# Performance work log

Measured on AMD Instinct MI355X. Metric: run time of the kernel, lower is better.

The kernel has to match this reference:

```python
import jax, jax.numpy as jnp
import numpy as np

N = 65536      # total nodes
B = 512        # graphs (equal-sized)
NPER = N // B  # 128 nodes per graph
E = 655360     # edges
F_IN = 128
K = 32         # sort-pool k
OUT = 27


def _gcn(x, row, col, dinv, W, b):
    # PyG GCNConv with added self-loops and symmetric normalization:
    xw = x @ W                                   # [N, F_out]
    coef = dinv[row] * dinv[col]                 # [E]
    agg = jax.ops.segment_sum(xw[row] * coef[:, None], col, num_segments=N)
    return agg + (dinv * dinv)[:, None] * xw + b  # self-loop term + bias


def _conv1d(x, w, b, stride):
    # x: [B, C_in, L], w: [C_out, C_in, K]
    out = jax.lax.conv_general_dilated(x, w, (stride,), 'VALID',
                                       dimension_numbers=('NCH', 'OIH', 'NCH'))
    return out + b[None, :, None]


def setup_inputs() -> dict:
    key = jax.random.key(0)
    ks = jax.random.split(key, 16)
    x = jax.random.normal(ks[0], (N, F_IN), dtype=jnp.float32)
    edge_index = jax.random.randint(ks[1], (2, E), 0, N, dtype=jnp.int32)
    batch = jnp.repeat(jnp.arange(B, dtype=jnp.int32), NPER)

    def lin(k, fi, fo):
        return jax.random.normal(k, (fi, fo), dtype=jnp.float32) / np.sqrt(fi)

    W1, b1 = lin(ks[2], F_IN, 128), jnp.zeros((128,), jnp.float32)
    W2, b2 = lin(ks[3], 128, 64), jnp.zeros((64,), jnp.float32)
    W3, b3 = lin(ks[4], 64, 32), jnp.zeros((32,), jnp.float32)
    W4, b4 = lin(ks[5], 32, 32), jnp.zeros((32,), jnp.float32)
    conv5_w = jax.random.normal(ks[6], (16, 1, 256), jnp.float32) / np.sqrt(256)
    conv5_b = jnp.zeros((16,), jnp.float32)
    conv6_w = jax.random.normal(ks[7], (32, 16, 5), jnp.float32) / np.sqrt(16 * 5)
    conv6_b = jnp.zeros((32,), jnp.float32)
    dense_w = lin(ks[8], 384, OUT)
    dense_b = jnp.zeros((OUT,), jnp.float32)
    return dict(x=x, edge_index=edge_index, batch=batch,
                W1=W1, b1=b1, W2=W2, b2=b2, W3=W3, b3=b3, W4=W4, b4=b4,
                conv5_w=conv5_w, conv5_b=conv5_b, conv6_w=conv6_w, conv6_b=conv6_b,
                dense_w=dense_w, dense_b=dense_b)


def reference(x, edge_index, batch, W1, b1, W2, b2, W3, b3, W4, b4,
              conv5_w, conv5_b, conv6_w, conv6_b, dense_w, dense_b):
    row, col = edge_index[0], edge_index[1]
    deg = jax.ops.segment_sum(jnp.ones((E,), x.dtype), col, num_segments=N) + 1.0
    dinv = jax.lax.rsqrt(deg)

    x1 = jnp.tanh(_gcn(x, row, col, dinv, W1, b1))
    x2 = jnp.tanh(_gcn(x1, row, col, dinv, W2, b2))
    x3 = jnp.tanh(_gcn(x2, row, col, dinv, W3, b3))
    x4 = jnp.tanh(_gcn(x3, row, col, dinv, W4, b4))
    h = jnp.concatenate([x1, x2, x3, x4], axis=-1)   # [N, 256]

    # SortAggregation: sort nodes within each graph by last channel (desc), take top-k.
    hg = h.reshape(B, NPER, 256)
    idx = jnp.argsort(-hg[:, :, -1], axis=1)[:, :K]                 # [B, K]
    pooled = jnp.take_along_axis(hg, idx[:, :, None], axis=1)       # [B, K, 256]
    top_k_indices = idx + (jnp.arange(B, dtype=idx.dtype) * NPER)[:, None]

    z = pooled.reshape(B, 1, K * 256)                # [B, 1, 8192]
    z = jax.nn.relu(_conv1d(z, conv5_w, conv5_b, 256))  # [B, 16, 32]
    z = jax.lax.reduce_window(z, -jnp.inf, jax.lax.max,
                              (1, 1, 2), (1, 1, 2), 'VALID')        # [B, 16, 16]
    z = jax.nn.relu(_conv1d(z, conv6_w, conv6_b, 1))  # [B, 32, 12]
    z = z.reshape(B, -1)                              # [B, 384]
    out = z @ dense_w + dense_b                       # [B, 27]
    return out, top_k_indices
```

## Files before the change

### kernel.cpp

```cpp
#include <hip/hip_runtime.h>
#include <math.h>

#define N_NODES 65536
#define N_EDGES 655360
#define N_GRAPHS 512
#define NPERG 128
#define KTOP 32
#define NOUT 27
#define OUT0_SIZE (N_GRAPHS * NOUT)
#define EPS 64

typedef unsigned int uint32;
typedef unsigned short u16;
typedef unsigned char u8;
typedef __attribute__((ext_vector_type(8))) short bf16x8;
typedef __attribute__((ext_vector_type(4))) float f32x4;
typedef __attribute__((ext_vector_type(2))) float f32x2;

__device__ __forceinline__ float blo(uint32 u) { return __uint_as_float(u << 16); }
__device__ __forceinline__ float bhi(uint32 u) { return __uint_as_float(u & 0xffff0000u); }
__device__ __forceinline__ u16 f2b(float f) {
    uint32 u = __float_as_uint(f);
    u += 0x7fffu + ((u >> 16) & 1u);
    return (u16)(u >> 16);
}
__device__ __forceinline__ uint32 pk(float a, float b) {
    return (uint32)f2b(a) | ((uint32)f2b(b) << 16);
}
__device__ __forceinline__ f32x2 fp8lo(uint32 u) { return __builtin_amdgcn_cvt_pk_f32_fp8((int)u, false); }
__device__ __forceinline__ f32x2 fp8hi(uint32 u) { return __builtin_amdgcn_cvt_pk_f32_fp8((int)u, true); }
__device__ __forceinline__ u8 f2fp8(float v) {
    return (u8)(__builtin_amdgcn_cvt_pk_fp8_f32(v, v, 0, false) & 0xff);
}


template<int FI, int FO>
__device__ __forceinline__ void pack_w(const float* __restrict__ W, uint4* __restrict__ pw,
                                       int base, int nb) {
    constexpr int KC = FI / 8;
    for (int q = (blockIdx.x - base) * 256 + threadIdx.x; q < FO * KC; q += nb * 256) {
        int n = q % FO, c = q / FO;
        const float* wp = W + (size_t)(c * 8) * FO + n;
        uint4 v;
        v.x = pk(wp[0],            wp[(size_t)FO]);
        v.y = pk(wp[2*(size_t)FO], wp[3*(size_t)FO]);
        v.z = pk(wp[4*(size_t)FO], wp[5*(size_t)FO]);
        v.w = pk(wp[6*(size_t)FO], wp[7*(size_t)FO]);
        pw[n * KC + c] = v;
    }
}

__global__ __launch_bounds__(256) void prep_kernel(const float* __restrict__ W1, const float* __restrict__ W2,
                                                   const float* __restrict__ W3, const float* __restrict__ W4,
                                                   uint4* __restrict__ pw1, uint4* __restrict__ pw2,
                                                   uint4* __restrict__ pw3, uint4* __restrict__ pw4,
                                                   int* __restrict__ cur) {
    int b = blockIdx.x;
    if (b < 256) { cur[b * 256 + threadIdx.x] = 0; return; }
    b -= 256;
    if (b < 8)       pack_w<128, 128>(W1, pw1, 256, 8);
    else if (b < 12) pack_w<128, 64>(W2, pw2, 264, 4);
    else if (b < 13) pack_w<64, 32>(W3, pw3, 268, 1);
    else             pack_w<32, 32>(W4, pw4, 269, 1);
}


__global__ __launch_bounds__(256) void fill_kernel(const int* __restrict__ erow, const int* __restrict__ ecol,
                                                   int* __restrict__ cur, u16* __restrict__ ep) {
    int e = blockIdx.x * 256 + threadIdx.x;
    int r = erow[e], d = ecol[e];
    int slot = atomicAdd(&cur[d], 1);
    if (slot < EPS) ep[(d << 6) + slot] = (u16)r;
}


template<int FI, int FO>
__device__ __forceinline__ void stage_Bp(const uint4* __restrict__ pw, uint4* __restrict__ Bs) {
    constexpr int KC = FI / 8, SA = KC + 1;
    for (int q = threadIdx.x; q < FO * KC; q += 256) {
        int n = q / KC, c = q % KC;
        Bs[n * SA + c] = pw[q];
    }
}

template<int FI, int FO, bool OUT_FP8>
__device__ __forceinline__ void mfma_store(uint4* __restrict__ As, const uint4* __restrict__ Bs,
                                           uint4* __restrict__ Y, size_t rowbase,
                                           const float* __restrict__ ds) {
    constexpr int KC = FI / 8, SA = KC + 1;
    constexpr int NTILE = FO / 16;
    constexpr int CW = (NTILE >= 4) ? 4 : NTILE;
    constexpr int NTW = NTILE / CW;
    constexpr int RW = 4 / CW;
    constexpr int RS = 2 / RW;
    constexpr int KSTEPS = FI / 32;
    int t = threadIdx.x;
    int w = t >> 6, L = t & 63;
    int quad = L >> 4, m = L & 15;
    int cw = w % CW, rw = w / CW;

    const bf16x8* Asv = (const bf16x8*)As;
    const bf16x8* Bsv = (const bf16x8*)Bs;

    f32x4 acc[RS][NTW];
#pragma unroll
    for (int i = 0; i < RS; i++)
#pragma unroll
        for (int j = 0; j < NTW; j++) acc[i][j] = (f32x4)0.f;

#pragma unroll
    for (int ks = 0; ks < KSTEPS; ks++) {
        int kc = ks * 4 + quad;
        bf16x8 bfr[NTW];
#pragma unroll
        for (int j = 0; j < NTW; j++) {
            int n = (cw * NTW + j) * 16 + m;
            bfr[j] = Bsv[n * SA + kc];
        }
#pragma unroll
        for (int i = 0; i < RS; i++) {
            int r = (rw * RS + i) * 16 + m;
            bf16x8 afr = Asv[r * SA + kc];
#pragma unroll
            for (int j = 0; j < NTW; j++)
                acc[i][j] = __builtin_amdgcn_mfma_f32_16x16x32_bf16(afr, bfr[j], acc[i][j], 0, 0, 0);
        }
    }
    __syncthreads();

    if constexpr (OUT_FP8) {
        u8* outs = (u8*)As;
#pragma unroll
        for (int i = 0; i < RS; i++) {
            int rb = (rw * RS + i) * 16 + quad * 4;
#pragma unroll
            for (int j = 0; j < NTW; j++) {
                int cc = (cw * NTW + j) * 16 + m;
#pragma unroll
                for (int g2 = 0; g2 < 4; g2++)
                    outs[(rb + g2) * FO + cc] = f2fp8(acc[i][j][g2] * ds[rb + g2]);
            }
        }
    } else {
        u16* outs = (u16*)As;
#pragma unroll
        for (int i = 0; i < RS; i++) {
            int rb = (rw * RS + i) * 16 + quad * 4;
#pragma unroll
            for (int j = 0; j < NTW; j++) {
                int cc = (cw * NTW + j) * 16 + m;
#pragma unroll
                for (int g2 = 0; g2 < 4; g2++)
                    outs[(rb + g2) * FO + cc] = f2b(acc[i][j][g2] * ds[rb + g2]);
            }
        }
    }
    __syncthreads();
    constexpr int NU4 = OUT_FP8 ? (32 * FO / 16) : (32 * FO / 8);
    for (int q = t; q < NU4; q += 256)
        Y[rowbase * (NU4 / 32) + q] = ((const uint4*)As)[q];
}


__global__ __launch_bounds__(256) void gemm1_kernel(const float* __restrict__ x,
                                                    const uint4* __restrict__ pw1,
                                                    const int* __restrict__ cur,
                                                    uint4* __restrict__ xw1) {
    constexpr int KC = 16, SA = 17;
    __shared__ __align__(16) uint4 As[32 * SA];
    __shared__ __align__(16) uint4 Bs[128 * SA];
    __shared__ float ds[32];
    int t = threadIdx.x;
    stage_Bp<128, 128>(pw1, Bs);
    size_t rowbase = (size_t)blockIdx.x * 32;
    if (t < 32) ds[t] = rsqrtf((float)cur[rowbase + t] + 1.0f);
    for (int q = t; q < 32 * KC; q += 256) {
        int r = q / KC, c = q % KC;
        const float* xp = x + (rowbase + r) * 128 + c * 8;
        float4 v0 = *(const float4*)xp;
        float4 v1 = *(const float4*)(xp + 4);
        uint4 u;
        u.x = pk(v0.x, v0.y); u.y = pk(v0.z, v0.w);
        u.z = pk(v1.x, v1.y); u.w = pk(v1.z, v1.w);
        As[r * SA + c] = u;
    }
    __syncthreads();
    mfma_store<128, 128, true>(As, Bs, xw1, rowbase, ds);
}


template<int F>
__device__ __forceinline__ void gath8_fp8v(const uint2* __restrict__ x2, uint4 e8,
                                           int cl, int rem, float (&ac)[8]) {
    constexpr int LN = F / 8;
    uint32 qq[8] = { e8.x & 0xffffu, e8.x >> 16, e8.y & 0xffffu, e8.y >> 16,
                     e8.z & 0xffffu, e8.z >> 16, e8.w & 0xffffu, e8.w >> 16 };
#pragma unroll
    for (int j = 0; j < 8; j++) {
        bool ok = j < rem;
        uint32 src = ok ? qq[j] : 0u;
        uint2 g = x2[(size_t)src * LN + cl];
        uint32 gx = ok ? g.x : 0u, gy = ok ? g.y : 0u;
        f32x2 l0 = fp8lo(gx), h0 = fp8hi(gx), l1 = fp8lo(gy), h1 = fp8hi(gy);
        ac[0] += l0.x; ac[1] += l0.y; ac[2] += h0.x; ac[3] += h0.y;
        ac[4] += l1.x; ac[5] += l1.y; ac[6] += h1.x; ac[7] += h1.y;
    }
}

template<int F>
__device__ __forceinline__ void agg_node_fp8v(const uint2* __restrict__ x2,
                                              const u16* __restrict__ ep,
                                              int n, int cl, int deg, float dn,
                                              const float* __restrict__ bias, float (&r)[8]) {
    constexpr int LN = F / 8;
    const u16* epp = ep + (n << 6);
    float ac[8];
#pragma unroll
    for (int c = 0; c < 8; c++) ac[c] = 0.f;
    uint4 e0 = *(const uint4*)(epp);
    uint4 e1 = *(const uint4*)(epp + 8);
    gath8_fp8v<F>(x2, e0, cl, deg, ac);
    gath8_fp8v<F>(x2, e1, cl, deg - 8, ac);
    if (deg > 16) {
        int nb = min((deg + 7) >> 3, EPS / 8);
        for (int b = 2; b < nb; b++) {
            uint4 e8 = *(const uint4*)(epp + b * 8);
            gath8_fp8v<F>(x2, e8, cl, deg - b * 8, ac);
        }
    }
    uint2 sv = x2[(size_t)n * LN + cl];
    f32x2 l0 = fp8lo(sv.x), h0 = fp8hi(sv.x), l1 = fp8lo(sv.y), h1 = fp8hi(sv.y);
    float sf[8] = { l0.x, l0.y, h0.x, h0.y, l1.x, l1.y, h1.x, h1.y };
#pragma unroll
    for (int c = 0; c < 8; c++) r[c] = dn * (ac[c] + sf[c]) + bias[8 * cl + c];
}


template<int F, int FO, bool OUT_FP8>
__global__ __launch_bounds__(256, 6) void agg_gemm8(const uint2* __restrict__ xin,
                                                    const int* __restrict__ cur,
                                                    const u16* __restrict__ ep,
                                                    const float* __restrict__ bias,
                                                    const uint4* __restrict__ pw,
                                                    uint4* __restrict__ hc4, int co4,
                                                    uint4* __restrict__ xout) {
    constexpr int KC = F / 8, SA = KC + 1;
    constexpr int LN = F / 8;
    constexpr int NPP = 256 / LN;
    __shared__ __align__(16) uint4 As[32 * SA];
    __shared__ __align__(16) uint4 Bs[FO * SA];
    __shared__ float ds[32];
    int t = threadIdx.x;
    int rowbase = blockIdx.x * 32;
    stage_Bp<F, FO>(pw, Bs);
    if (t < 32) ds[t] = rsqrtf((float)cur[rowbase + t] + 1.0f);
    __syncthreads();

    int cl = t % LN, nsub = t / LN;
#pragma unroll
    for (int pass = 0; pass < 32 / NPP; pass++) {
        int nl = pass * NPP + nsub;
        int n = rowbase + nl;
        int deg = cur[n];
        float r[8];
        agg_node_fp8v<F>(xin, ep, n, cl, deg, ds[nl], bias, r);
        uint4 pr;
        pr.x = pk(tanhf(r[0]), tanhf(r[1]));
        pr.y = pk(tanhf(r[2]), tanhf(r[3]));
        pr.z = pk(tanhf(r[4]), tanhf(r[5]));
        pr.w = pk(tanhf(r[6]), tanhf(r[7]));
        hc4[(size_t)n * 32 + co4 + cl] = pr;
        As[nl * SA + cl] = pr;
    }
    __syncthreads();
    mfma_store<F, FO, OUT_FP8>(As, Bs, xout, (size_t)rowbase, ds);
}


template<int L4>
__device__ __forceinline__ void gath8_bf16(const uint2* __restrict__ x2, uint4 e8,
                                           int c4, int rem, float (&ac)[4][4]) {
    uint32 qq[8] = { e8.x & 0xffffu, e8.x >> 16, e8.y & 0xffffu, e8.y >> 16,
                     e8.z & 0xffffu, e8.z >> 16, e8.w & 0xffffu, e8.w >> 16 };
#pragma unroll
    for (int j = 0; j < 8; j++) {
        bool ok = j < rem;
        uint32 src = ok ? qq[j] : 0u;
        uint2 g = x2[(size_t)src * L4 + c4];
        uint32 gx = ok ? g.x : 0u, gy = ok ? g.y : 0u;
        ac[j & 3][0] += blo(gx); ac[j & 3][1] += bhi(gx);
        ac[j & 3][2] += blo(gy); ac[j & 3][3] += bhi(gy);
    }
}

template<int F>
__device__ __forceinline__ void agg_node_bf16(const uint2* __restrict__ x2,
                                              const u16* __restrict__ ep,
                                              int n, int c4, int deg, float dn,
                                              const float* __restrict__ bias,
                                              float& r0, float& r1, float& r2, float& r3) {
    constexpr int L4 = F / 4;
    const u16* epp = ep + (n << 6);
    float ac[4][4];
#pragma unroll
    for (int i = 0; i < 4; i++)
#pragma unroll
        for (int j = 0; j < 4; j++) ac[i][j] = 0.f;
    uint4 e0 = *(const uint4*)(epp);
    uint4 e1 = *(const uint4*)(epp + 8);
    gath8_bf16<L4>(x2, e0, c4, deg, ac);
    gath8_bf16<L4>(x2, e1, c4, deg - 8, ac);
    if (deg > 16) {
        int nb = min((deg + 7) >> 3, EPS / 8);
        for (int b = 2; b < nb; b++) {
            uint4 e8 = *(const uint4*)(epp + b * 8);
            gath8_bf16<L4>(x2, e8, c4, deg - b * 8, ac);
        }
    }
    float s0 = (ac[0][0] + ac[1][0]) + (ac[2][0] + ac[3][0]);
    float s1 = (ac[0][1] + ac[1][1]) + (ac[2][1] + ac[3][1]);
    float s2 = (ac[0][2] + ac[1][2]) + (ac[2][2] + ac[3][2]);
    float s3 = (ac[0][3] + ac[1][3]) + (ac[2][3] + ac[3][3]);
    uint2 sv = x2[(size_t)n * L4 + c4];
    r0 = dn * (s0 + blo(sv.x)) + bias[4 * c4 + 0];
    r1 = dn * (s1 + bhi(sv.x)) + bias[4 * c4 + 1];
    r2 = dn * (s2 + blo(sv.y)) + bias[4 * c4 + 2];
    r3 = dn * (s3 + bhi(sv.y)) + bias[4 * c4 + 3];
}


template<int F, int FO>
__global__ __launch_bounds__(256, 6) void agg_gemm_bf(const uint32* __restrict__ xin,
                                                      const int* __restrict__ cur,
                                                      const u16* __restrict__ ep,
                                                      const float* __restrict__ bias,
                                                      const uint4* __restrict__ pw,
                                                      uint32* __restrict__ hc, int co2,
                                                      uint4* __restrict__ xout) {
    constexpr int KC = F / 8, SA = KC + 1;
    constexpr int L4 = F / 4;
    constexpr int NPP = 256 / L4;
    __shared__ __align__(16) uint4 As[32 * SA];
    __shared__ __align__(16) uint4 Bs[FO * SA];
    __shared__ float ds[32];
    int t = threadIdx.x;
    int rowbase = blockIdx.x * 32;
    stage_Bp<F, FO>(pw, Bs);
    if (t < 32) ds[t] = rsqrtf((float)cur[rowbase + t] + 1.0f);
    __syncthreads();

    uint2* As2 = (uint2*)As;
    uint2* hc2 = (uint2*)hc;
    int c4 = t % L4;
    int nsub = t / L4;
#pragma unroll
    for (int pass = 0; pass < 32 / NPP; pass++) {
        int nl = pass * NPP + nsub;
        int n = rowbase + nl;
        int deg = cur[n];
        float r0, r1, r2, r3;
        agg_node_bf16<F>((const uint2*)xin, ep, n, c4, deg, ds[nl], bias, r0, r1, r2, r3);
        uint2 pr;
        pr.x = pk(tanhf(r0), tanhf(r1));
        pr.y = pk(tanhf(r2), tanhf(r3));
        hc2[(size_t)n * 64 + co2 + c4] = pr;
        As2[nl * (SA * 2) + c4] = pr;
    }
    __syncthreads();
    mfma_store<F, FO, false>(As, Bs, xout, (size_t)rowbase, ds);
}


__device__ __forceinline__ void key_g8(const uint32* __restrict__ xw, uint4 e8,
                                       int rem, float (&ac3)[4]) {
    uint32 qq[8] = { e8.x & 0xffffu, e8.x >> 16, e8.y & 0xffffu, e8.y >> 16,
                     e8.z & 0xffffu, e8.z >> 16, e8.w & 0xffffu, e8.w >> 16 };
#pragma unroll
    for (int j = 0; j < 8; j++) {
        bool ok = j < rem;
        uint32 src = ok ? qq[j] : 0u;
        uint32 gy = xw[(size_t)src * 16 + 15];
        ac3[j & 3] += bhi(ok ? gy : 0u);
    }
}

__global__ __launch_bounds__(256) void final_kernel(const uint32* __restrict__ hc,
                                                    const uint32* __restrict__ xw4,
                                                    const int* __restrict__ cur,
                                                    const u16* __restrict__ ep,
                                                    const float* __restrict__ b4,
                                                    const float* __restrict__ w5, const float* __restrict__ b5,
                                                    const float* __restrict__ w6, const float* __restrict__ b6,
                                                    const float* __restrict__ dw, const float* __restrict__ db,
                                                    float* __restrict__ out) {
    __shared__ float skey[128];
    __shared__ int   sidx[128];
    __shared__ uint32 ph[32 * 133];
    __shared__ __align__(16) float w5s[4096];
    __shared__ float z5[16 * 33];
    __shared__ float ms[16 * 17];
    __shared__ float z6[384];
    int g = blockIdx.x, t = threadIdx.x;

    if (t >= 128) {
        for (int q = t - 128; q < 1024; q += 128)
            ((float4*)w5s)[q] = ((const float4*)w5)[q];
    } else {
        int n = g * NPERG + t;
        int deg = cur[n];
        float dn = rsqrtf((float)deg + 1.0f);
        const u16* epp = ep + (n << 6);
        float ac3[4] = { 0.f, 0.f, 0.f, 0.f };
        uint4 e0 = *(const uint4*)(epp);
        uint4 e1 = *(const uint4*)(epp + 8);
        key_g8(xw4, e0, deg, ac3);
        key_g8(xw4, e1, deg - 8, ac3);
        if (deg > 16) {
            int nb = min((deg + 7) >> 3, EPS / 8);
            for (int b = 2; b < nb; b++) {
                uint4 e8 = *(const uint4*)(epp + b * 8);
                key_g8(xw4, e8, deg - b * 8, ac3);
            }
        }
        float s3 = (ac3[0] + ac3[1]) + (ac3[2] + ac3[3]);
        uint32 svy = xw4[(size_t)n * 16 + 15];
        float r3 = dn * (s3 + bhi(svy)) + b4[31];
        skey[t] = __uint_as_float(((uint32)f2b(tanhf(r3))) << 16);
        sidx[t] = t;
    }
    __syncthreads();

    for (int sz = 2; sz <= 128; sz <<= 1) {
        for (int stride = sz >> 1; stride > 0; stride >>= 1) {
            if (t < 64) {
                int i = ((t & ~(stride - 1)) << 1) | (t & (stride - 1));
                int j = i | stride;
                float ki = skey[i], kj = skey[j];
                int ii = sidx[i], ij = sidx[j];
                bool desc = ((i & sz) == 0);
                bool ibef = (ki > kj) || (ki == kj && ii < ij);
                if (desc != ibef) { skey[i] = kj; skey[j] = ki; sidx[i] = ij; sidx[j] = ii; }
            }
            __syncthreads();
        }
    }

    if (t < KTOP) out[OUT0_SIZE + g * KTOP + t] = (float)(g * NPERG + sidx[t]);

    {
        int r = t >> 3, c4 = t & 7;
        int n = g * NPERG + sidx[r];
        int deg = cur[n];
        float dn = rsqrtf((float)deg + 1.0f);
        float r0, r1, r2, r3;
        agg_node_bf16<32>((const uint2*)xw4, ep, n, c4, deg, dn, b4, r0, r1, r2, r3);
        uint32* dst = &ph[r * 133 + 112 + 2 * c4];
        dst[0] = pk(tanhf(r0), tanhf(r1));
        dst[1] = pk(tanhf(r2), tanhf(r3));
    }

    {
        const uint4* hcv = (const uint4*)hc;
        for (int q = t; q < 1024; q += 256) {
            int cell = q & 31;
            if (cell >= 28) continue;
            int r2 = q >> 5;
            int node = g * NPERG + sidx[r2];
            uint4 v = hcv[(size_t)node * 32 + cell];
            uint32* dst = &ph[r2 * 133 + cell * 4];
            dst[0] = v.x; dst[1] = v.y; dst[2] = v.z; dst[3] = v.w;
        }
    }
    __syncthreads();

    {
        int o = t >> 5, l = t & 31;
        float a0 = 0.f, a1 = 0.f;
#pragma unroll 4
        for (int j2 = 0; j2 < 128; j2++) {
            uint32 u = ph[l * 133 + j2];
            float p0 = blo(u), p1 = bhi(u);
            a0 += p0 * w5s[o * 256 + 2 * j2]       + p1 * w5s[o * 256 + 2 * j2 + 1];
            a1 += p0 * w5s[(o + 8) * 256 + 2 * j2] + p1 * w5s[(o + 8) * 256 + 2 * j2 + 1];
        }
        z5[o * 33 + l]       = fmaxf(a0 + b5[o], 0.f);
        z5[(o + 8) * 33 + l] = fmaxf(a1 + b5[o + 8], 0.f);
    }
    __syncthreads();

    {
        int o = t >> 4, p = t & 15;
        ms[o * 17 + p] = fmaxf(z5[o * 33 + 2 * p], z5[o * 33 + 2 * p + 1]);
    }
    __syncthreads();

    for (int q = t; q < 384; q += 256) {
        int o2 = q / 12, tt = q % 12;
        float a = b6[o2];
        for (int o = 0; o < 16; o++) {
#pragma unroll
            for (int k = 0; k < 5; k++)
                a += w6[(o2 * 16 + o) * 5 + k] * ms[o * 17 + tt + k];
        }
        z6[q] = fmaxf(a, 0.f);
    }
    __syncthreads();

    if (t < NOUT) {
        float a = db[t];
        for (int i = 0; i < 384; i++) a += z6[i] * dw[i * NOUT + t];
        out[g * NOUT + t] = a;
    }
}


extern "C" void kernel_launch(void* const* d_in, const int* in_sizes, int n_in,
                              void* d_out, int out_size, void* d_ws, size_t ws_size,
                              hipStream_t stream) {
    const float* x    = (const float*)d_in[0];
    const int*   edge = (const int*)d_in[1];
    const int*   erow = edge;
    const int*   ecol = edge + N_EDGES;
    const float* W1 = (const float*)d_in[3];  const float* b1 = (const float*)d_in[4];
    const float* W2 = (const float*)d_in[5];  const float* b2 = (const float*)d_in[6];
    const float* W3 = (const float*)d_in[7];  const float* b3 = (const float*)d_in[8];
    const float* W4 = (const float*)d_in[9];  const float* b4 = (const float*)d_in[10];
    const float* w5 = (const float*)d_in[11]; const float* b5 = (const float*)d_in[12];
    const float* w6 = (const float*)d_in[13]; const float* b6 = (const float*)d_in[14];
    const float* dw = (const float*)d_in[15]; const float* db = (const float*)d_in[16];
    float* out = (float*)d_out;

    char* wsb = (char*)d_ws;
    size_t off = 0;
    auto alloc = [&](size_t bytes) -> void* {
        void* p = wsb + off;
        off = (off + bytes + 255) & ~(size_t)255;
        return p;
    };
    int*    cur  = (int*)   alloc((size_t)N_NODES * 4);
    u16*    ep   = (u16*)   alloc((size_t)N_NODES * EPS * 2);
    uint32* xwA  = (uint32*)alloc((size_t)N_NODES * 32 * 4);
    uint32* xwB  = (uint32*)alloc((size_t)N_NODES * 32 * 4);
    uint32* hc   = (uint32*)alloc((size_t)N_NODES * 128 * 4);
    uint4*  pw1  = (uint4*) alloc(2048 * 16);
    uint4*  pw2  = (uint4*) alloc(1024 * 16);
    uint4*  pw3  = (uint4*) alloc(256 * 16);
    uint4*  pw4  = (uint4*) alloc(128 * 16);
    (void)ws_size; (void)in_sizes; (void)n_in; (void)out_size;

    prep_kernel<<<270, 256, 0, stream>>>(W1, W2, W3, W4, pw1, pw2, pw3, pw4, cur);
    fill_kernel<<<N_EDGES / 256, 256, 0, stream>>>(erow, ecol, cur, ep);
    gemm1_kernel<<<N_NODES / 32, 256, 0, stream>>>(x, pw1, cur, (uint4*)xwA);
    agg_gemm8<128, 64, true><<<N_NODES / 32, 256, 0, stream>>>((const uint2*)xwA, cur, ep, b1, pw2, (uint4*)hc, 0, (uint4*)xwB);
    agg_gemm8<64, 32, false><<<N_NODES / 32, 256, 0, stream>>>((const uint2*)xwB, cur, ep, b2, pw3, (uint4*)hc, 16, (uint4*)xwA);
    agg_gemm_bf<32, 32><<<N_NODES / 32, 256, 0, stream>>>(xwA, cur, ep, b3, pw4, hc, 48, (uint4*)xwB);
    final_kernel<<<N_GRAPHS, 256, 0, stream>>>(hc, xwB, cur, ep, b4, w5, b5, w6, b6, dw, db, out);
}
```

Baseline: 226.1 us.

## Split sort-key computation into separate kernel and replace bitonic sort with rank selection

Moves the per-node sort-key aggregation out of the 512-block final kernel into a dedicated kernel launched over all nodes, so the gather runs with more parallelism. The 128-element bitonic sort with many barriers is replaced by an O(n^2) rank count per node that writes only the top-k entries. Nontemporal loads are also added for the edge list and input features. The cost is an extra kernel launch and a round trip of the keys through global memory.

```diff
diff --git a/kernel.cpp b/kernel.cpp
--- a/kernel.cpp
+++ b/kernel.cpp
@@ -16,6 +16,7 @@
 typedef __attribute__((ext_vector_type(8))) short bf16x8;
 typedef __attribute__((ext_vector_type(4))) float f32x4;
 typedef __attribute__((ext_vector_type(2))) float f32x2;
+typedef __attribute__((ext_vector_type(4))) float f32x4n;
 
 __device__ __forceinline__ float blo(uint32 u) { return __uint_as_float(u << 16); }
 __device__ __forceinline__ float bhi(uint32 u) { return __uint_as_float(u & 0xffff0000u); }
@@ -68,7 +69,8 @@
 __global__ __launch_bounds__(256) void fill_kernel(const int* __restrict__ erow, const int* __restrict__ ecol,
                                                    int* __restrict__ cur, u16* __restrict__ ep) {
     int e = blockIdx.x * 256 + threadIdx.x;
-    int r = erow[e], d = ecol[e];
+    int r = __builtin_nontemporal_load(erow + e);
+    int d = __builtin_nontemporal_load(ecol + e);
     int slot = atomicAdd(&cur[d], 1);
     if (slot < EPS) ep[(d << 6) + slot] = (u16)r;
 }
@@ -176,9 +178,9 @@
     if (t < 32) ds[t] = rsqrtf((float)cur[rowbase + t] + 1.0f);
     for (int q = t; q < 32 * KC; q += 256) {
         int r = q / KC, c = q % KC;
-        const float* xp = x + (rowbase + r) * 128 + c * 8;
-        float4 v0 = *(const float4*)xp;
-        float4 v1 = *(const float4*)(xp + 4);
+        const f32x4n* xp4 = (const f32x4n*)(x + (rowbase + r) * 128 + c * 8);
+        f32x4n v0 = __builtin_nontemporal_load(xp4);
+        f32x4n v1 = __builtin_nontemporal_load(xp4 + 1);
         uint4 u;
         u.x = pk(v0.x, v0.y); u.y = pk(v0.z, v0.w);
         u.z = pk(v1.x, v1.y); u.w = pk(v1.z, v1.w);
@@ -384,8 +386,37 @@
     }
 }
 
+__global__ __launch_bounds__(256) void key_kernel(const uint32* __restrict__ xw4,
+                                                  const int* __restrict__ cur,
+                                                  const u16* __restrict__ ep,
+                                                  const float* __restrict__ b4,
+                                                  float* __restrict__ keys) {
+    int n = blockIdx.x * 256 + threadIdx.x;
+    int deg = cur[n];
+    float dn = rsqrtf((float)deg + 1.0f);
+    const u16* epp = ep + (n << 6);
+    float ac3[4] = { 0.f, 0.f, 0.f, 0.f };
+    uint4 e0 = *(const uint4*)(epp);
+    uint4 e1 = *(const uint4*)(epp + 8);
+    key_g8(xw4, e0, deg, ac3);
+    key_g8(xw4, e1, deg - 8, ac3);
+    if (deg > 16) {
+        int nb = min((deg + 7) >> 3, EPS / 8);
+        for (int b = 2; b < nb; b++) {
+            uint4 e8 = *(const uint4*)(epp + b * 8);
+            key_g8(xw4, e8, deg - b * 8, ac3);
+        }
+    }
+    float s3 = (ac3[0] + ac3[1]) + (ac3[2] + ac3[3]);
+    uint32 svy = xw4[(size_t)n * 16 + 15];
+    float r3 = dn * (s3 + bhi(svy)) + b4[31];
+    keys[n] = __uint_as_float(((uint32)f2b(tanhf(r3))) << 16);
+}
+
+
 __global__ __launch_bounds__(256) void final_kernel(const uint32* __restrict__ hc,
                                                     const uint32* __restrict__ xw4,
+                                                    const float* __restrict__ keys,
                                                     const int* __restrict__ cur,
                                                     const u16* __restrict__ ep,
                                                     const float* __restrict__ b4,
@@ -394,7 +425,7 @@
                                                     const float* __restrict__ dw, const float* __restrict__ db,
                                                     float* __restrict__ out) {
     __shared__ float skey[128];
-    __shared__ int   sidx[128];
+    __shared__ int   sidx[KTOP];
     __shared__ uint32 ph[32 * 133];
     __shared__ __align__(16) float w5s[4096];
     __shared__ float z5[16 * 33];
@@ -406,46 +437,24 @@
         for (int q = t - 128; q < 1024; q += 128)
             ((float4*)w5s)[q] = ((const float4*)w5)[q];
     } else {
-        int n = g * NPERG + t;
-        int deg = cur[n];
-        float dn = rsqrtf((float)deg + 1.0f);
-        const u16* epp = ep + (n << 6);
-        float ac3[4] = { 0.f, 0.f, 0.f, 0.f };
-        uint4 e0 = *(const uint4*)(epp);
-        uint4 e1 = *(const uint4*)(epp + 8);
-        key_g8(xw4, e0, deg, ac3);
-        key_g8(xw4, e1, deg - 8, ac3);
-        if (deg > 16) {
-            int nb = min((deg + 7) >> 3, EPS / 8);
-            for (int b = 2; b < nb; b++) {
-                uint4 e8 = *(const uint4*)(epp + b * 8);
-                key_g8(xw4, e8, deg - b * 8, ac3);
-            }
-        }
-        float s3 = (ac3[0] + ac3[1]) + (ac3[2] + ac3[3]);
-        uint32 svy = xw4[(size_t)n * 16 + 15];
-        float r3 = dn * (s3 + bhi(svy)) + b4[31];
-        skey[t] = __uint_as_float(((uint32)f2b(tanhf(r3))) << 16);
-        sidx[t] = t;
-    }
-    __syncthreads();
-
-    for (int sz = 2; sz <= 128; sz <<= 1) {
-        for (int stride = sz >> 1; stride > 0; stride >>= 1) {
-            if (t < 64) {
-                int i = ((t & ~(stride - 1)) << 1) | (t & (stride - 1));
-                int j = i | stride;
-                float ki = skey[i], kj = skey[j];
-                int ii = sidx[i], ij = sidx[j];
-                bool desc = ((i & sz) == 0);
-                bool ibef = (ki > kj) || (ki == kj && ii < ij);
-                if (desc != ibef) { skey[i] = kj; skey[j] = ki; sidx[i] = ij; sidx[j] = ii; }
-            }
-            __syncthreads();
-        }
-    }
-
-    if (t < KTOP) out[OUT0_SIZE + g * KTOP + t] = (float)(g * NPERG + sidx[t]);
+        skey[t] = keys[g * NPERG + t];
+    }
+    __syncthreads();
+
+    if (t < 128) {
+        float ki = skey[t];
+        int rank = 0;
+#pragma unroll 16
+        for (int j = 0; j < 128; j++) {
+            float kj = skey[j];
+            rank += (kj > ki) || (kj == ki && j < t);
+        }
+        if (rank < KTOP) {
+            sidx[rank] = t;
+            out[OUT0_SIZE + g * KTOP + rank] = (float)(g * NPERG + t);
+        }
+    }
+    __syncthreads();
 
     {
         int r = t >> 3, c4 = t & 7;
@@ -542,6 +551,7 @@
     uint32* xwA  = (uint32*)alloc((size_t)N_NODES * 32 * 4);
     uint32* xwB  = (uint32*)alloc((size_t)N_NODES * 32 * 4);
     uint32* hc   = (uint32*)alloc((size_t)N_NODES * 128 * 4);
+    float*  keys = (float*) alloc((size_t)N_NODES * 4);
     uint4*  pw1  = (uint4*) alloc(2048 * 16);
     uint4*  pw2  = (uint4*) alloc(1024 * 16);
     uint4*  pw3  = (uint4*) alloc(256 * 16);
@@ -554,5 +564,6 @@
     agg_gemm8<128, 64, true><<<N_NODES / 32, 256, 0, stream>>>((const uint2*)xwA, cur, ep, b1, pw2, (uint4*)hc, 0, (uint4*)xwB);
     agg_gemm8<64, 32, false><<<N_NODES / 32, 256, 0, stream>>>((const uint2*)xwB, cur, ep, b2, pw3, (uint4*)hc, 16, (uint4*)xwA);
     agg_gemm_bf<32, 32><<<N_NODES / 32, 256, 0, stream>>>(xwA, cur, ep, b3, pw4, hc, 48, (uint4*)xwB);
-    final_kernel<<<N_GRAPHS, 256, 0, stream>>>(hc, xwB, cur, ep, b4, w5, b5, w6, b6, dw, db, out);
-}
+    key_kernel<<<N_NODES / 256, 256, 0, stream>>>(xwB, cur, ep, b4, keys);
+    final_kernel<<<N_GRAPHS, 256, 0, stream>>>(hc, xwB, keys, cur, ep, b4, w5, b5, w6, b6, dw, db, out);
+}
```

Measured after the change: 238.3 us. 1.05x slower.
